# Performance work log

Measured on AMD Instinct MI355X. Metric: run time of the kernel, lower is better.

The kernel has to match this reference:

```python
import jax, jax.numpy as jnp
import numpy as np

GROUPS = 8   # GroupNorm groups used by create_pat_conv*_blocks(..., groups=8)
EPS = 1e-5
K = 20       # num_neighbor


def group_norm(x, gamma, beta):
    # x: [B, C, ...spatial]
    B, C = x.shape[0], x.shape[1]
    shape = x.shape
    xg = x.reshape(B, GROUPS, C // GROUPS, -1)
    m = xg.mean(axis=(2, 3), keepdims=True)
    v = ((xg - m) ** 2).mean(axis=(2, 3), keepdims=True)
    xg = (xg - m) * jax.lax.rsqrt(v + EPS)
    x = xg.reshape(shape)
    bshape = (1, C) + (1,) * (len(shape) - 2)
    return x * gamma.reshape(bshape) + beta.reshape(bshape)


def conv_block(x, w, b, gamma, beta):
    # pointwise (kernel-size 1) conv + GroupNorm + ELU, works for 1d and 2d spatial
    y = jnp.einsum('oc,bc...->bo...', w, x) + b.reshape((1, -1) + (1,) * (x.ndim - 2))
    return jax.nn.elu(group_norm(y, gamma, beta))


def knn_graph(points, k):
    # points: [B, 3, N] -> neighbor coords [B, 3, N, k] (self included, dilation=1)
    sq = jnp.sum(points * points, axis=1)                      # [B, N]
    inner = jnp.einsum('bci,bcj->bij', points, points)         # [B, N, N]
    dist = sq[:, :, None] + sq[:, None, :] - 2.0 * inner       # squared pairwise dist
    _, idx = jax.lax.top_k(-dist, k)                           # [B, N, k] smallest dists
    neighbors = jnp.take_along_axis(points[:, :, None, :], idx[:, None, :, :], axis=3)
    return neighbors                                           # [B, 3, N, k]


def setup_inputs() -> dict:
    key = jax.random.key(0)
    B, N = 4, 8192
    dims1 = [6, 32, 64]
    dims2 = [64, 512, 1024]
    keys = iter(jax.random.split(key, 32))
    inp = {"points": jax.random.normal(next(keys), (B, 3, N), dtype=jnp.float32)}
    for tag, dims in (("p1", dims1), ("p2", dims2)):
        for i in range(len(dims) - 1):
            cin, cout = dims[i], dims[i + 1]
            inp[f"{tag}_w{i}"] = jax.random.normal(next(keys), (cout, cin), dtype=jnp.float32) / np.float32(np.sqrt(cin))
            inp[f"{tag}_b{i}"] = jnp.zeros((cout,), dtype=jnp.float32)
            inp[f"{tag}_g{i}"] = jnp.ones((cout,), dtype=jnp.float32)
            inp[f"{tag}_beta{i}"] = jnp.zeros((cout,), dtype=jnp.float32)
    return inp


def reference(points, p1_w0, p1_b0, p1_g0, p1_beta0, p1_w1, p1_b1, p1_g1, p1_beta1,
              p2_w0, p2_b0, p2_g0, p2_beta0, p2_w1, p2_b1, p2_g1, p2_beta1):
    neighbors = knn_graph(points, K)                             # [B, 3, N, K]
    center = jnp.broadcast_to(points[:, :, :, None], neighbors.shape)
    x = jnp.concatenate([center, neighbors - center], axis=1)   # [B, 6, N, K]
    x = conv_block(x, p1_w0, p1_b0, p1_g0, p1_beta0)            # [B, 32, N, K]
    x = conv_block(x, p1_w1, p1_b1, p1_g1, p1_beta1)            # [B, 64, N, K]
    x = jnp.max(x, axis=2)                                      # [B, 64, K] (faithful to source: max over dim=2)
    x = conv_block(x, p2_w0, p2_b0, p2_g0, p2_beta0)            # [B, 512, K]
    x = conv_block(x, p2_w1, p2_b1, p2_g1, p2_beta1)            # [B, 1024, K]
    return x
```

## Files before the change

### kernel.cpp

```cpp
#include <hip/hip_runtime.h>
#include <math.h>

#define NPTS   8192
#define BATCH  4
#define KNN    20
#define NKTOT  (NPTS*KNN)
#define EPS    1e-5f
#define TILE3  1024
#define QCAP   64

typedef float v2f __attribute__((ext_vector_type(2)));

__device__ __forceinline__ float elu(float x) { return x > 0.0f ? x : expm1f(x); }
__device__ __forceinline__ float eluf(float x) { return x > 0.0f ? x : __expf(x) - 1.0f; }
__device__ __forceinline__ v2f splat2(float x) { v2f v; v.x = x; v.y = x; return v; }
__device__ __forceinline__ float rfl(float x) {
    return __uint_as_float(__builtin_amdgcn_readfirstlane(__float_as_uint(x)));
}

__device__ __forceinline__ unsigned fenc(float f) {
    unsigned b = __float_as_uint(f);
    return b ^ ((unsigned)(((int)b) >> 31) | 0x80000000u);
}
__device__ __forceinline__ float fdec(unsigned u) {
    unsigned b = (u & 0x80000000u) ? (u ^ 0x80000000u) : ~u;
    return __uint_as_float(b);
}

__global__ __launch_bounds__(256) void prep_kernel(const float* __restrict__ points,
                                                   float4* __restrict__ pts4)
{
    const int t = blockIdx.x * 256 + threadIdx.x;
    const int b = t >> 13, n = t & (NPTS - 1);
    const float* px = points + b * 3 * NPTS;
    float x = px[n], y = px[NPTS + n], z = px[2 * NPTS + n];
    pts4[t] = make_float4(x, y, z, -0.5f * (x * x + y * y + z * z));
}

__global__ __launch_bounds__(256, 4) void knn_kernel(const float4* __restrict__ pts4,
                                                     int* __restrict__ idx_out)
{
    __shared__ __align__(16) float4 tileS[TILE3];
    __shared__ unsigned long long queue[32][QCAP];
    __shared__ int qcnt[32];

    const int tid  = threadIdx.x;
    const int lane = tid & 63;
    const int wv   = tid >> 6;
    const int b    = blockIdx.x >> 8;
    const int q0   = (blockIdx.x & 255) * 32 + wv * 8;
    const float4* pb = pts4 + b * NPTS;

    float qx[8], qy[8], qz[8];
    v2f smax2[8];
#pragma unroll
    for (int q = 0; q < 8; ++q) {
        float4 qp = pb[q0 + q];
        qx[q] = rfl(qp.x); qy[q] = rfl(qp.y); qz[q] = rfl(qp.z);
        smax2[q] = splat2(-INFINITY);
    }
    if (tid < 32) qcnt[tid] = 0;

    for (int t = 0; t < NPTS / TILE3; ++t) {
        __syncthreads();
        for (int i = tid; i < TILE3; i += 256) tileS[i] = pb[t * TILE3 + i];
        __syncthreads();
#pragma unroll 4
        for (int s = 0; s < TILE3 / 128; ++s) {
            float4 p0 = tileS[s * 128 + lane];
            float4 p1 = tileS[s * 128 + 64 + lane];
            v2f px = { p0.x, p1.x }, py = { p0.y, p1.y };
            v2f pz = { p0.z, p1.z }, pw = { p0.w, p1.w };
#pragma unroll
            for (int q = 0; q < 8; ++q) {
                v2f sv = __builtin_elementwise_fma(splat2(qx[q]), px,
                         __builtin_elementwise_fma(splat2(qy[q]), py,
                         __builtin_elementwise_fma(splat2(qz[q]), pz, pw)));
                smax2[q] = __builtin_elementwise_max(smax2[q], sv);
            }
        }
    }

    float sgate[8];
#pragma unroll
    for (int q = 0; q < 8; ++q) {
        float v = fmaxf(smax2[q].x, smax2[q].y);
#pragma unroll
        for (int k = 2; k <= 64; k <<= 1)
#pragma unroll
            for (int j = k >> 1; j >= 1; j >>= 1) {
                float o = __shfl_xor(v, j);
                bool up = ((lane & k) == 0);
                bool keepmin = (((lane & j) == 0) == up);
                v = keepmin ? fminf(v, o) : fmaxf(v, o);
            }
        float m = __shfl(v, 44);
        sgate[q] = m - 1e-4f - 1e-5f * fabsf(m);
    }

    for (int t = 0; t < NPTS / TILE3; ++t) {
        __syncthreads();
        for (int i = tid; i < TILE3; i += 256) tileS[i] = pb[t * TILE3 + i];
        __syncthreads();
        for (int s = 0; s < TILE3 / 128; ++s) {
            float4 p0 = tileS[s * 128 + lane];
            float4 p1 = tileS[s * 128 + 64 + lane];
            v2f px = { p0.x, p1.x }, py = { p0.y, p1.y };
            v2f pz = { p0.z, p1.z }, pw = { p0.w, p1.w };
            const int jb = t * TILE3 + s * 128;
#pragma unroll
            for (int q = 0; q < 8; ++q) {
                v2f sv = __builtin_elementwise_fma(splat2(qx[q]), px,
                         __builtin_elementwise_fma(splat2(qy[q]), py,
                         __builtin_elementwise_fma(splat2(qz[q]), pz, pw)));
#pragma unroll
                for (int h = 0; h < 2; ++h) {
                    float svh = h ? sv.y : sv.x;
                    if (svh >= sgate[q]) {
                        int slot = atomicAdd(&qcnt[wv * 8 + q], 1);
                        if (slot < QCAP) {
                            unsigned long long key =
                                ((unsigned long long)fenc(svh) << 32)
                                | (unsigned)(NPTS - 1 - (jb + h * 64 + lane));
                            queue[wv * 8 + q][slot] = key;
                        }
                    }
                }
            }
        }
    }
    __syncthreads();

#pragma unroll
    for (int q = 0; q < 8; ++q) {
        const int cq = qcnt[wv * 8 + q];
        unsigned long long key = (lane < cq) ? queue[wv * 8 + q][lane] : 0ull;
#pragma unroll
        for (int k = 2; k <= 64; k <<= 1)
#pragma unroll
            for (int j = k >> 1; j >= 1; j >>= 1) {
                unsigned long long o = __shfl_xor(key, j);
                bool up = ((lane & k) == 0);
                bool keepmax = (((lane & j) == 0) == up);
                bool omax = o > key;
                key = (keepmax == omax) ? o : key;
            }
        if (lane < KNN)
            idx_out[(b * NPTS + q0 + q) * KNN + lane] =
                NPTS - 1 - (int)(unsigned)(key & 0xFFFFFFFFu);
    }
}

__global__ __launch_bounds__(256) void moments_x_kernel(const float* __restrict__ points,
                                                        const int* __restrict__ idx,
                                                        float* __restrict__ sums1p)
{
    const int t = blockIdx.x * 256 + threadIdx.x;
    const int b = blockIdx.x / 640;
    const int r = t - b * NKTOT;
    const int n = r / KNN;
    const float* px = points + b * 3 * NPTS;
    const int j = idx[t];
    float cx = px[n], cy = px[NPTS + n], cz = px[2 * NPTS + n];
    float v[27];
    v[0] = cx; v[1] = cy; v[2] = cz;
    v[3] = px[j] - cx; v[4] = px[NPTS + j] - cy; v[5] = px[2 * NPTS + j] - cz;
    int p = 6;
#pragma unroll
    for (int d = 0; d < 6; ++d)
#pragma unroll
        for (int e = d; e < 6; ++e) v[p++] = v[d] * v[e];
#pragma unroll
    for (int i = 0; i < 27; ++i)
        for (int o = 32; o > 0; o >>= 1) v[i] += __shfl_xor(v[i], o);

    __shared__ float red[4][27];
    const int lane = threadIdx.x & 63, w = threadIdx.x >> 6;
    if (lane == 0)
#pragma unroll
        for (int i = 0; i < 27; ++i) red[w][i] = v[i];
    __syncthreads();
    if (threadIdx.x < 27) {
        float acc = red[0][threadIdx.x] + red[1][threadIdx.x] + red[2][threadIdx.x] + red[3][threadIdx.x];
        int slot = blockIdx.x & 63;
        atomicAdd(&sums1p[(slot * BATCH + b) * 27 + threadIdx.x], acc);
    }
}

__global__ void finalize1_kernel(const float* __restrict__ sums1p,
                                 const float* __restrict__ w1, const float* __restrict__ b1,
                                 const float* __restrict__ g1, const float* __restrict__ beta1,
                                 float* __restrict__ w1f)
{
    __shared__ float S[BATCH][27];
    const int t = threadIdx.x;
    if (t < 108) {
        int b = t / 27, i = t % 27;
        float acc = 0.f;
        for (int s = 0; s < 64; ++s) acc += sums1p[(s * BATCH + b) * 27 + i];
        S[b][i] = acc;
    }
    __syncthreads();
    const int b = t >> 5, c = t & 31;
    const float invS = 1.0f / (float)NKTOT;
    float Ex[6], M[6][6];
#pragma unroll
    for (int d = 0; d < 6; ++d) Ex[d] = S[b][d] * invS;
    int p = 6;
#pragma unroll
    for (int d = 0; d < 6; ++d)
#pragma unroll
        for (int e = d; e < 6; ++e) { float v = S[b][p++] * invS; M[d][e] = v; M[e][d] = v; }
    const int g = c >> 2;
    float msum = 0.f, qsum = 0.f;
    for (int cc = g * 4; cc < g * 4 + 4; ++cc) {
        float w[6];
#pragma unroll
        for (int d = 0; d < 6; ++d) w[d] = w1[cc * 6 + d];
        float dotEx = 0.f;
#pragma unroll
        for (int d = 0; d < 6; ++d) dotEx += w[d] * Ex[d];
        float Ey = dotEx + b1[cc];
        float Ey2 = 0.f;
#pragma unroll
        for (int d = 0; d < 6; ++d)
#pragma unroll
            for (int e = 0; e < 6; ++e) Ey2 += w[d] * w[e] * M[d][e];
        Ey2 += 2.0f * b1[cc] * dotEx + b1[cc] * b1[cc];
        msum += Ey; qsum += Ey2;
    }
    float m = msum * 0.25f;
    float var = qsum * 0.25f - m * m;
    float inv = rsqrtf(var + EPS);
    float s = g1[c] * inv;
    float tt = s * (b1[c] - m) + beta1[c];
    float* o = w1f + (b * 32 + c) * 8;
#pragma unroll
    for (int d = 0; d < 6; ++d) o[d] = s * w1[c * 6 + d];
    o[6] = tt; o[7] = 0.f;
}

__global__ __launch_bounds__(256, 5) void fused_main_kernel(
    const float4* __restrict__ pts4, const int* __restrict__ idxb,
    const float* __restrict__ w1f, const float* __restrict__ w2, const float* __restrict__ b2,
    float* __restrict__ sums2p, unsigned int* __restrict__ maxenc, unsigned int* __restrict__ minenc)
{
    __shared__ __align__(16) float w2t[32 * 64];
    __shared__ __align__(16) float z1s[32 * 64];
    __shared__ __align__(16) float4 w1s4[64];
    __shared__ float b2s[64];
    __shared__ float redmx[64], redmn[64], sqred[32];

    const int t   = threadIdx.x;
    const int blk = blockIdx.x;
    const int nc  = blk & 15;
    const int k   = (blk >> 4) % 20;
    const int b   = blk / 320;

    for (int i = t; i < 512; i += 256) {
        float4 v = ((const float4*)w2)[i];
        int c = i >> 3, kq = (i & 7) * 4;
        w2t[(kq + 0) * 64 + c] = v.x; w2t[(kq + 1) * 64 + c] = v.y;
        w2t[(kq + 2) * 64 + c] = v.z; w2t[(kq + 3) * 64 + c] = v.w;
    }
    if (t < 64) { w1s4[t] = ((const float4*)w1f)[b * 64 + t]; b2s[t] = b2[t]; }

    const int ln   = t & 63;
    const int cg   = t >> 6;
    const int pos0 = (t & 15) * 4;
    const int c0   = (t >> 4) * 4;
    const float4* pb = pts4 + b * NPTS;
    const int nbase = nc * 512;

    float mx[4], mn[4];
#pragma unroll
    for (int ci = 0; ci < 4; ++ci) { mx[ci] = -INFINITY; mn[ci] = INFINITY; }
    float gs = 0.f, gq = 0.f;

    for (int st = 0; st < 8; ++st) {
        const int n = nbase + st * 64 + ln;
        const int j = idxb[(b * NPTS + n) * KNN + k];
        float4 c4 = pb[n];
        float4 e4 = pb[j];
        float x0[6] = { c4.x, c4.y, c4.z, e4.x - c4.x, e4.y - c4.y, e4.z - c4.z };

        __syncthreads();
#pragma unroll
        for (int jj = 0; jj < 8; ++jj) {
            int c = cg * 8 + jj;
            float4 wA = w1s4[c * 2 + 0];
            float4 wB = w1s4[c * 2 + 1];
            float z = wB.z;
            z = fmaf(wA.x, x0[0], z); z = fmaf(wA.y, x0[1], z); z = fmaf(wA.z, x0[2], z);
            z = fmaf(wA.w, x0[3], z); z = fmaf(wB.x, x0[4], z); z = fmaf(wB.y, x0[5], z);
            z1s[c * 64 + ln] = eluf(z);
        }
        __syncthreads();

        float acc[4][4];
#pragma unroll
        for (int ci = 0; ci < 4; ++ci) {
            float bb = b2s[c0 + ci];
#pragma unroll
            for (int pj = 0; pj < 4; ++pj) acc[ci][pj] = bb;
        }
#pragma unroll
        for (int kk = 0; kk < 32; ++kk) {
            float4 av = *(const float4*)&w2t[kk * 64 + c0];
            float4 bv = *(const float4*)&z1s[kk * 64 + pos0];
            float avv[4] = { av.x, av.y, av.z, av.w };
            float bvv[4] = { bv.x, bv.y, bv.z, bv.w };
#pragma unroll
            for (int ci = 0; ci < 4; ++ci)
#pragma unroll
                for (int pj = 0; pj < 4; ++pj) acc[ci][pj] = fmaf(avv[ci], bvv[pj], acc[ci][pj]);
        }
#pragma unroll
        for (int ci = 0; ci < 4; ++ci)
#pragma unroll
            for (int pj = 0; pj < 4; ++pj) {
                float v = acc[ci][pj];
                gs += v; gq = fmaf(v, v, gq);
                mx[ci] = fmaxf(mx[ci], v); mn[ci] = fminf(mn[ci], v);
            }
    }

#pragma unroll
    for (int m = 1; m <= 8; m <<= 1) {
#pragma unroll
        for (int ci = 0; ci < 4; ++ci) {
            mx[ci] = fmaxf(mx[ci], __shfl_xor(mx[ci], m));
            mn[ci] = fminf(mn[ci], __shfl_xor(mn[ci], m));
        }
        gs += __shfl_xor(gs, m);
        gq += __shfl_xor(gq, m);
    }
    if ((t & 15) == 0) {
        int qd = t >> 4;
#pragma unroll
        for (int ci = 0; ci < 4; ++ci) { redmx[qd * 4 + ci] = mx[ci]; redmn[qd * 4 + ci] = mn[ci]; }
        sqred[qd * 2 + 0] = gs; sqred[qd * 2 + 1] = gq;
    }
    __syncthreads();
    if (t < 64) {
        atomicMax(&maxenc[(b * 64 + t) * KNN + k], fenc(redmx[t]));
    } else if (t < 128) {
        int c = t - 64;
        atomicMin(&minenc[(b * 64 + c) * KNN + k], fenc(redmn[c]));
    } else if (t < 144) {
        int i2 = t - 128, g = i2 >> 1, w = i2 & 1;
        float v = sqred[(2 * g) * 2 + w] + sqred[(2 * g + 1) * 2 + w];
        int slot = blk & 63;
        atomicAdd(&sums2p[((slot * BATCH + b) * 8 + g) * 2 + w], v);
    }
}

__global__ void build_m1_kernel(const float* __restrict__ sums2p,
                                const unsigned int* __restrict__ maxenc,
                                const unsigned int* __restrict__ minenc,
                                const float* __restrict__ gamma, const float* __restrict__ beta,
                                float* __restrict__ m1)
{
    const int t = blockIdx.x * 256 + threadIdx.x;
    const int b = t / 1280;
    const int r = t - b * 1280;
    const int c = r / 20;
    const int g = c >> 3;
    float s = 0.f, q = 0.f;
    for (int sl = 0; sl < 64; ++sl) {
        s += sums2p[((sl * BATCH + b) * 8 + g) * 2 + 0];
        q += sums2p[((sl * BATCH + b) * 8 + g) * 2 + 1];
    }
    const float cnt = 8.0f * (float)NKTOT;
    float m = s / cnt;
    float var = q / cnt - m * m;
    float inv = rsqrtf(var + EPS);
    float sc = gamma[c] * inv;
    float tt = beta[c] - sc * m;
    float y = (sc >= 0.f) ? fdec(maxenc[t]) : fdec(minenc[t]);
    m1[t] = elu(sc * y + tt);
}

template <int CIN, int SLOTS>
__global__ void p2_gemm_kernel(const float* __restrict__ zin, const float* __restrict__ w,
                               const float* __restrict__ bias, float* __restrict__ yout,
                               float* __restrict__ sumsp, int chans_per_group)
{
    const int t = blockIdx.x * 256 + threadIdx.x;
    const int per_b = (gridDim.x * 256) / BATCH;
    const int b = t / per_b;
    const int r = t - b * per_b;
    const int o = r / 20;
    const int k = r - o * 20;
    const float* zb = zin + b * CIN * 20;
    const float* wrow = w + o * CIN;
    float acc = bias[o];
    for (int c = 0; c < CIN; c += 4) {
        float4 wv = *(const float4*)&wrow[c];
        acc += wv.x * zb[(c + 0) * 20 + k] + wv.y * zb[(c + 1) * 20 + k]
             + wv.z * zb[(c + 2) * 20 + k] + wv.w * zb[(c + 3) * 20 + k];
    }
    yout[t] = acc;

    __shared__ float ls[16];
    if (threadIdx.x < 16) ls[threadIdx.x] = 0.f;
    __syncthreads();
    const int g = o / chans_per_group;
    atomicAdd(&ls[g * 2 + 0], acc);
    atomicAdd(&ls[g * 2 + 1], acc * acc);
    __syncthreads();
    if (threadIdx.x < 16) {
        int slot = blockIdx.x & (SLOTS - 1);
        atomicAdd(&sumsp[(slot * BATCH + b) * 16 + threadIdx.x], ls[threadIdx.x]);
    }
}

template <int SLOTS>
__global__ void p2_finalize_kernel(const float* __restrict__ y, const float* __restrict__ sumsp,
                                   const float* __restrict__ gamma, const float* __restrict__ beta,
                                   float* __restrict__ z, int chans_per_group, float cnt)
{
    const int t = blockIdx.x * 256 + threadIdx.x;
    const int per_b = (gridDim.x * 256) / BATCH;
    const int b = t / per_b;
    const int r = t - b * per_b;
    const int o = r / 20;
    const int g = o / chans_per_group;
    float s = 0.f, q = 0.f;
    for (int sl = 0; sl < SLOTS; ++sl) {
        s += sumsp[(sl * BATCH + b) * 16 + g * 2 + 0];
        q += sumsp[(sl * BATCH + b) * 16 + g * 2 + 1];
    }
    float m = s / cnt;
    float var = q / cnt - m * m;
    float inv = rsqrtf(var + EPS);
    float v = gamma[o] * inv * (y[t] - m) + beta[o];
    z[t] = elu(v);
}

extern "C" void kernel_launch(void* const* d_in, const int* in_sizes, int n_in,
                              void* d_out, int out_size, void* d_ws, size_t ws_size,
                              hipStream_t stream)
{
    const float* points  = (const float*)d_in[0];
    const float* p1_w0   = (const float*)d_in[1];
    const float* p1_b0   = (const float*)d_in[2];
    const float* p1_g0   = (const float*)d_in[3];
    const float* p1_bt0  = (const float*)d_in[4];
    const float* p1_w1   = (const float*)d_in[5];
    const float* p1_b1   = (const float*)d_in[6];
    const float* p1_g1   = (const float*)d_in[7];
    const float* p1_bt1  = (const float*)d_in[8];
    const float* p2_w0   = (const float*)d_in[9];
    const float* p2_b0   = (const float*)d_in[10];
    const float* p2_g0   = (const float*)d_in[11];
    const float* p2_bt0  = (const float*)d_in[12];
    const float* p2_w1   = (const float*)d_in[13];
    const float* p2_b1   = (const float*)d_in[14];
    const float* p2_g1   = (const float*)d_in[15];
    const float* p2_bt1  = (const float*)d_in[16];
    float* out = (float*)d_out;

    float* ws = (float*)d_ws;
    int*      idx     = (int*)ws;
    float*    sums1p  = ws + 655360;
    float*    sums2p  = sums1p + 6912;
    float*    sumsAp  = sums2p + 4096;
    float*    sumsBp  = sumsAp + 1024;
    unsigned* maxenc  = (unsigned*)(sumsBp + 1024);
    unsigned* minenc  = maxenc + 5120;
    float*    w1f     = (float*)(minenc + 5120);
    float*    m1      = w1f + 1024;
    float*    yp2a    = m1 + 5120;
    float*    zp2a    = yp2a + 40960;
    float*    yp2b    = zp2a + 40960;
    float4*   pts4    = (float4*)yp2a;

    hipMemsetAsync(sums1p, 0, (6912 + 4096 + 1024 + 1024 + 5120) * sizeof(float), stream);
    hipMemsetAsync(minenc, 0xFF, 5120 * sizeof(unsigned), stream);

    prep_kernel<<<128, 256, 0, stream>>>(points, pts4);
    knn_kernel<<<1024, 256, 0, stream>>>(pts4, idx);
    moments_x_kernel<<<2560, 256, 0, stream>>>(points, idx, sums1p);
    finalize1_kernel<<<1, 128, 0, stream>>>(sums1p, p1_w0, p1_b0, p1_g0, p1_bt0, w1f);
    fused_main_kernel<<<1280, 256, 0, stream>>>(pts4, idx, w1f, p1_w1, p1_b1,
                                                sums2p, maxenc, minenc);
    build_m1_kernel<<<20, 256, 0, stream>>>(sums2p, maxenc, minenc, p1_g1, p1_bt1, m1);
    p2_gemm_kernel<64, 16><<<160, 256, 0, stream>>>(m1, p2_w0, p2_b0, yp2a, sumsAp, 64);
    p2_finalize_kernel<16><<<160, 256, 0, stream>>>(yp2a, sumsAp, p2_g0, p2_bt0, zp2a, 64, 1280.0f);
    p2_gemm_kernel<512, 16><<<320, 256, 0, stream>>>(zp2a, p2_w1, p2_b1, yp2b, sumsBp, 128);
    p2_finalize_kernel<16><<<320, 256, 0, stream>>>(yp2b, sumsBp, p2_g1, p2_bt1, out, 128, 2560.0f);
}
```

Measured before the change: 296.6 us.

## Restructure KNN kernel with larger SoA tiles, register prefetch, 512-thread blocks

The KNN kernel now uses 512-thread blocks covering 64 queries and loads 2048-point tiles in structure-of-arrays shared layout, so each lane reads contiguous v2f pairs. The next tile is prefetched from global memory into registers while the current tile is computed, hiding load latency behind the FMA loop. The candidate queue shrinks to 48 entries and the count is clamped before the final sort. Shared memory per block grows and the smaller queue cap raises the risk of overflow when many candidates pass the gate.

```diff
diff --git a/kernel.cpp b/kernel.cpp
--- a/kernel.cpp
+++ b/kernel.cpp
@@ -6,8 +6,8 @@
 #define KNN    20
 #define NKTOT  (NPTS*KNN)
 #define EPS    1e-5f
-#define TILE3  1024
-#define QCAP   64
+#define TILE4  2048
+#define QCAP   48
 
 typedef float v2f __attribute__((ext_vector_type(2)));
 
@@ -37,19 +37,21 @@
     pts4[t] = make_float4(x, y, z, -0.5f * (x * x + y * y + z * z));
 }
 
-__global__ __launch_bounds__(256, 4) void knn_kernel(const float4* __restrict__ pts4,
+__global__ __launch_bounds__(512, 4) void knn_kernel(const float4* __restrict__ pts4,
                                                      int* __restrict__ idx_out)
 {
-    __shared__ __align__(16) float4 tileS[TILE3];
-    __shared__ unsigned long long queue[32][QCAP];
-    __shared__ int qcnt[32];
+    __shared__ float tx[TILE4], ty[TILE4], tz[TILE4], tw[TILE4];
+    __shared__ unsigned long long queue[64][QCAP];
+    __shared__ int qcnt[64];
 
     const int tid  = threadIdx.x;
     const int lane = tid & 63;
     const int wv   = tid >> 6;
-    const int b    = blockIdx.x >> 8;
-    const int q0   = (blockIdx.x & 255) * 32 + wv * 8;
+    const int b    = blockIdx.x >> 7;
+    const int q0   = (blockIdx.x & 127) * 64 + wv * 8;
     const float4* pb = pts4 + b * NPTS;
+
+    if (tid < 64) qcnt[tid] = 0;
 
     float qx[8], qy[8], qz[8];
     v2f smax2[8];
@@ -59,18 +61,29 @@
         qx[q] = rfl(qp.x); qy[q] = rfl(qp.y); qz[q] = rfl(qp.z);
         smax2[q] = splat2(-INFINITY);
     }
-    if (tid < 32) qcnt[tid] = 0;
-
-    for (int t = 0; t < NPTS / TILE3; ++t) {
+
+    float4 pf[4];
+#pragma unroll
+    for (int r = 0; r < 4; ++r) pf[r] = pb[tid + r * 512];
+
+    for (int t = 0; t < NPTS / TILE4; ++t) {
         __syncthreads();
-        for (int i = tid; i < TILE3; i += 256) tileS[i] = pb[t * TILE3 + i];
+#pragma unroll
+        for (int r = 0; r < 4; ++r) {
+            int i = tid + r * 512;
+            tx[i] = pf[r].x; ty[i] = pf[r].y; tz[i] = pf[r].z; tw[i] = pf[r].w;
+        }
         __syncthreads();
-#pragma unroll 4
-        for (int s = 0; s < TILE3 / 128; ++s) {
-            float4 p0 = tileS[s * 128 + lane];
-            float4 p1 = tileS[s * 128 + 64 + lane];
-            v2f px = { p0.x, p1.x }, py = { p0.y, p1.y };
-            v2f pz = { p0.z, p1.z }, pw = { p0.w, p1.w };
+        if (t + 1 < NPTS / TILE4) {
+#pragma unroll
+            for (int r = 0; r < 4; ++r) pf[r] = pb[(t + 1) * TILE4 + tid + r * 512];
+        }
+#pragma unroll 2
+        for (int s = 0; s < TILE4 / 128; ++s) {
+            v2f px = *(const v2f*)&tx[s * 128 + 2 * lane];
+            v2f py = *(const v2f*)&ty[s * 128 + 2 * lane];
+            v2f pz = *(const v2f*)&tz[s * 128 + 2 * lane];
+            v2f pw = *(const v2f*)&tw[s * 128 + 2 * lane];
 #pragma unroll
             for (int q = 0; q < 8; ++q) {
                 v2f sv = __builtin_elementwise_fma(splat2(qx[q]), px,
@@ -80,6 +93,9 @@
             }
         }
     }
+
+#pragma unroll
+    for (int r = 0; r < 4; ++r) pf[r] = pb[tid + r * 512];
 
     float sgate[8];
 #pragma unroll
@@ -98,16 +114,24 @@
         sgate[q] = m - 1e-4f - 1e-5f * fabsf(m);
     }
 
-    for (int t = 0; t < NPTS / TILE3; ++t) {
+    for (int t = 0; t < NPTS / TILE4; ++t) {
         __syncthreads();
-        for (int i = tid; i < TILE3; i += 256) tileS[i] = pb[t * TILE3 + i];
+#pragma unroll
+        for (int r = 0; r < 4; ++r) {
+            int i = tid + r * 512;
+            tx[i] = pf[r].x; ty[i] = pf[r].y; tz[i] = pf[r].z; tw[i] = pf[r].w;
+        }
         __syncthreads();
-        for (int s = 0; s < TILE3 / 128; ++s) {
-            float4 p0 = tileS[s * 128 + lane];
-            float4 p1 = tileS[s * 128 + 64 + lane];
-            v2f px = { p0.x, p1.x }, py = { p0.y, p1.y };
-            v2f pz = { p0.z, p1.z }, pw = { p0.w, p1.w };
-            const int jb = t * TILE3 + s * 128;
+        if (t + 1 < NPTS / TILE4) {
+#pragma unroll
+            for (int r = 0; r < 4; ++r) pf[r] = pb[(t + 1) * TILE4 + tid + r * 512];
+        }
+        for (int s = 0; s < TILE4 / 128; ++s) {
+            v2f px = *(const v2f*)&tx[s * 128 + 2 * lane];
+            v2f py = *(const v2f*)&ty[s * 128 + 2 * lane];
+            v2f pz = *(const v2f*)&tz[s * 128 + 2 * lane];
+            v2f pw = *(const v2f*)&tw[s * 128 + 2 * lane];
+            const int jb = t * TILE4 + s * 128 + 2 * lane;
 #pragma unroll
             for (int q = 0; q < 8; ++q) {
                 v2f sv = __builtin_elementwise_fma(splat2(qx[q]), px,
@@ -121,7 +145,7 @@
                         if (slot < QCAP) {
                             unsigned long long key =
                                 ((unsigned long long)fenc(svh) << 32)
-                                | (unsigned)(NPTS - 1 - (jb + h * 64 + lane));
+                                | (unsigned)(NPTS - 1 - (jb + h));
                             queue[wv * 8 + q][slot] = key;
                         }
                     }
@@ -133,7 +157,7 @@
 
 #pragma unroll
     for (int q = 0; q < 8; ++q) {
-        const int cq = qcnt[wv * 8 + q];
+        int cq = qcnt[wv * 8 + q]; cq = cq < QCAP ? cq : QCAP;
         unsigned long long key = (lane < cq) ? queue[wv * 8 + q][lane] : 0ull;
 #pragma unroll
         for (int k = 2; k <= 64; k <<= 1)
@@ -480,7 +504,7 @@
     hipMemsetAsync(minenc, 0xFF, 5120 * sizeof(unsigned), stream);
 
     prep_kernel<<<128, 256, 0, stream>>>(points, pts4);
-    knn_kernel<<<1024, 256, 0, stream>>>(pts4, idx);
+    knn_kernel<<<512, 512, 0, stream>>>(pts4, idx);
     moments_x_kernel<<<2560, 256, 0, stream>>>(points, idx, sums1p);
     finalize1_kernel<<<1, 128, 0, stream>>>(sums1p, p1_w0, p1_b0, p1_g0, p1_bt0, w1f);
     fused_main_kernel<<<1280, 256, 0, stream>>>(pts4, idx, w1f, p1_w1, p1_b1,
```

After: 294.1 us. About the same (-0.8%).

## Drop shared-memory tiling in kNN kernel, read points directly from global

Applied to the files above, without the earlier changes.

Removes the LDS tile and the per-tile __syncthreads in both kNN passes. Each wave now streams point pairs straight from global memory (and L2) with interleaved lane indexing, so waves run independently. The candidate queue is shrunk to 40 entries and the occupancy hint is raised to 8 blocks, with the queue count clamped when read. It also adds a combined max pre-check before the per-half gate test. Risks are heavier global/L2 traffic per wave and possible overflow of the smaller queue, which could drop true neighbours if more than 40 candidates pass the gate.

```diff
diff --git a/kernel.cpp b/kernel.cpp
--- a/kernel.cpp
+++ b/kernel.cpp
@@ -6,8 +6,7 @@
 #define KNN    20
 #define NKTOT  (NPTS*KNN)
 #define EPS    1e-5f
-#define TILE3  1024
-#define QCAP   64
+#define QCAP   40
 
 typedef float v2f __attribute__((ext_vector_type(2)));
 
@@ -37,10 +36,9 @@
     pts4[t] = make_float4(x, y, z, -0.5f * (x * x + y * y + z * z));
 }
 
-__global__ __launch_bounds__(256, 4) void knn_kernel(const float4* __restrict__ pts4,
+__global__ __launch_bounds__(256, 8) void knn_kernel(const float4* __restrict__ pts4,
                                                      int* __restrict__ idx_out)
 {
-    __shared__ __align__(16) float4 tileS[TILE3];
     __shared__ unsigned long long queue[32][QCAP];
     __shared__ int qcnt[32];
 
@@ -51,6 +49,8 @@
     const int q0   = (blockIdx.x & 255) * 32 + wv * 8;
     const float4* pb = pts4 + b * NPTS;
 
+    if (lane < 8) qcnt[wv * 8 + lane] = 0;
+
     float qx[8], qy[8], qz[8];
     v2f smax2[8];
 #pragma unroll
@@ -59,25 +59,19 @@
         qx[q] = rfl(qp.x); qy[q] = rfl(qp.y); qz[q] = rfl(qp.z);
         smax2[q] = splat2(-INFINITY);
     }
-    if (tid < 32) qcnt[tid] = 0;
-
-    for (int t = 0; t < NPTS / TILE3; ++t) {
-        __syncthreads();
-        for (int i = tid; i < TILE3; i += 256) tileS[i] = pb[t * TILE3 + i];
-        __syncthreads();
+
 #pragma unroll 4
-        for (int s = 0; s < TILE3 / 128; ++s) {
-            float4 p0 = tileS[s * 128 + lane];
-            float4 p1 = tileS[s * 128 + 64 + lane];
-            v2f px = { p0.x, p1.x }, py = { p0.y, p1.y };
-            v2f pz = { p0.z, p1.z }, pw = { p0.w, p1.w };
-#pragma unroll
-            for (int q = 0; q < 8; ++q) {
-                v2f sv = __builtin_elementwise_fma(splat2(qx[q]), px,
-                         __builtin_elementwise_fma(splat2(qy[q]), py,
-                         __builtin_elementwise_fma(splat2(qz[q]), pz, pw)));
-                smax2[q] = __builtin_elementwise_max(smax2[q], sv);
-            }
+    for (int t = 0; t < NPTS / 128; ++t) {
+        float4 p0 = pb[t * 128 + 2 * lane];
+        float4 p1 = pb[t * 128 + 2 * lane + 1];
+        v2f px = { p0.x, p1.x }, py = { p0.y, p1.y };
+        v2f pz = { p0.z, p1.z }, pw = { p0.w, p1.w };
+#pragma unroll
+        for (int q = 0; q < 8; ++q) {
+            v2f sv = __builtin_elementwise_fma(splat2(qx[q]), px,
+                     __builtin_elementwise_fma(splat2(qy[q]), py,
+                     __builtin_elementwise_fma(splat2(qz[q]), pz, pw)));
+            smax2[q] = __builtin_elementwise_max(smax2[q], sv);
         }
     }
 
@@ -98,21 +92,19 @@
         sgate[q] = m - 1e-4f - 1e-5f * fabsf(m);
     }
 
-    for (int t = 0; t < NPTS / TILE3; ++t) {
-        __syncthreads();
-        for (int i = tid; i < TILE3; i += 256) tileS[i] = pb[t * TILE3 + i];
-        __syncthreads();
-        for (int s = 0; s < TILE3 / 128; ++s) {
-            float4 p0 = tileS[s * 128 + lane];
-            float4 p1 = tileS[s * 128 + 64 + lane];
-            v2f px = { p0.x, p1.x }, py = { p0.y, p1.y };
-            v2f pz = { p0.z, p1.z }, pw = { p0.w, p1.w };
-            const int jb = t * TILE3 + s * 128;
-#pragma unroll
-            for (int q = 0; q < 8; ++q) {
-                v2f sv = __builtin_elementwise_fma(splat2(qx[q]), px,
-                         __builtin_elementwise_fma(splat2(qy[q]), py,
-                         __builtin_elementwise_fma(splat2(qz[q]), pz, pw)));
+#pragma unroll 2
+    for (int t = 0; t < NPTS / 128; ++t) {
+        float4 p0 = pb[t * 128 + 2 * lane];
+        float4 p1 = pb[t * 128 + 2 * lane + 1];
+        v2f px = { p0.x, p1.x }, py = { p0.y, p1.y };
+        v2f pz = { p0.z, p1.z }, pw = { p0.w, p1.w };
+        const int jb = t * 128 + 2 * lane;
+#pragma unroll
+        for (int q = 0; q < 8; ++q) {
+            v2f sv = __builtin_elementwise_fma(splat2(qx[q]), px,
+                     __builtin_elementwise_fma(splat2(qy[q]), py,
+                     __builtin_elementwise_fma(splat2(qz[q]), pz, pw)));
+            if (fmaxf(sv.x, sv.y) >= sgate[q]) {
 #pragma unroll
                 for (int h = 0; h < 2; ++h) {
                     float svh = h ? sv.y : sv.x;
@@ -121,7 +113,7 @@
                         if (slot < QCAP) {
                             unsigned long long key =
                                 ((unsigned long long)fenc(svh) << 32)
-                                | (unsigned)(NPTS - 1 - (jb + h * 64 + lane));
+                                | (unsigned)(NPTS - 1 - (jb + h));
                             queue[wv * 8 + q][slot] = key;
                         }
                     }
@@ -129,11 +121,10 @@
             }
         }
     }
-    __syncthreads();
 
 #pragma unroll
     for (int q = 0; q < 8; ++q) {
-        const int cq = qcnt[wv * 8 + q];
+        int cq = qcnt[wv * 8 + q]; cq = cq < QCAP ? cq : QCAP;
         unsigned long long key = (lane < cq) ? queue[wv * 8 + q][lane] : 0ull;
 #pragma unroll
         for (int k = 2; k <= 64; k <<= 1)
```

Result: no change. 295.2 us (-0.5%).
